# Kernel optimization log

Measured on AMD Instinct MI355X. Metric: run time of the kernel, lower is better.

## Reference

```python
import jax, jax.numpy as jnp
import numpy as np

D = 4096       # hidden_size
H = 32         # n_heads (tp_size=1)
DN = 128       # qk_nope_head_dim
DR = 64        # qk_rope_head_dim
DV = 128       # v_head_dim
QL = 1536      # q_lora_rank
KL = 512       # kv_lora_rank
S = 2048       # seqlen, start_pos = 0
EPS = 1e-6
SCALE = (DN + DR) ** -0.5  # softmax_scale (no yarn mscale: seqlen <= original_seq_len)
THETA = 10000.0


def _freqs(seqlen, dim, base=THETA):
    # precompute_freqs_cis without yarn correction (seqlen <= original_seq_len)
    inv = 1.0 / (base ** (np.arange(0, dim, 2, dtype=np.float32) / dim))
    f = np.outer(np.arange(seqlen, dtype=np.float32), inv)  # [S, dim//2]
    return jnp.asarray(np.cos(f)), jnp.asarray(np.sin(f))


def _rmsnorm(x, w):
    return x * jax.lax.rsqrt(jnp.mean(x * x, axis=-1, keepdims=True) + EPS) * w


def _rope(x, cos, sin):
    # x: [S, H, R]; complex rotation on consecutive pairs (view_as_complex semantics)
    S_, H_, R_ = x.shape
    xr = x.reshape(S_, H_, R_ // 2, 2)
    x0, x1 = xr[..., 0], xr[..., 1]
    c = cos[:, None, :]
    s = sin[:, None, :]
    y0 = x0 * c - x1 * s
    y1 = x0 * s + x1 * c
    return jnp.stack([y0, y1], axis=-1).reshape(S_, H_, R_)


def setup_inputs() -> dict:
    key = jax.random.key(0)
    ks = jax.random.split(key, 6)
    std = 0.02
    return {
        "x": jax.random.normal(ks[0], (S, D), jnp.float32),
        "wq_a": jax.random.normal(ks[1], (QL, D), jnp.float32) * std,
        "q_norm_w": jnp.ones((QL,), jnp.float32),
        "wq_b": jax.random.normal(ks[2], (H * (DN + DR), QL), jnp.float32) * std,
        "wkv_a": jax.random.normal(ks[3], (KL + DR, D), jnp.float32) * std,
        "kv_norm_w": jnp.ones((KL,), jnp.float32),
        "wkv_b": jax.random.normal(ks[4], (H * (DN + DV), KL), jnp.float32) * std,
        "wo": jax.random.normal(ks[5], (D, H * DV), jnp.float32) * std,
    }


def reference(x, wq_a, q_norm_w, wq_b, wkv_a, kv_norm_w, wkv_b, wo):
    cos, sin = _freqs(S, DR)

    # q path: low-rank down-proj + RMSNorm + up-proj
    q = _rmsnorm(x @ wq_a.T, q_norm_w) @ wq_b.T          # [S, H*(DN+DR)]
    q = q.reshape(S, H, DN + DR)
    q_nope, q_pe = q[..., :DN], q[..., DN:]
    q_pe = _rope(q_pe, cos, sin)                          # [S, H, DR]

    # kv path: joint latent + rope part
    kv_all = x @ wkv_a.T                                  # [S, KL+DR]
    kv = _rmsnorm(kv_all[:, :KL], kv_norm_w)              # latent kv cache [S, KL]
    k_pe = _rope(kv_all[:, None, KL:], cos, sin)[:, 0, :]  # pe cache [S, DR]

    # absorb k-up-projection into q (einsum 'shd,hdc->shc')
    wkv_b_r = wkv_b.reshape(H, DN + DV, KL)
    q_lat = jnp.einsum("shd,hdc->shc", q_nope, wkv_b_r[:, :DN])  # [S, H, KL]

    scores = (jnp.einsum("shc,tc->sht", q_lat, kv)
              + jnp.einsum("shr,tr->sht", q_pe, k_pe)) * SCALE   # [S, H, T]

    causal = jnp.arange(S)[:, None] >= jnp.arange(S)[None, :]     # [S, T]
    scores = jnp.where(causal[:, None, :], scores, -jnp.inf)
    p = jax.nn.softmax(scores, axis=-1)

    o_lat = jnp.einsum("sht,tc->shc", p, kv)                      # [S, H, KL]
    o = jnp.einsum("shc,hdc->shd", o_lat, wkv_b_r[:, DN:])        # [S, H, DV]
    return o.reshape(S, H * DV) @ wo.T                            # [S, D]
```

## Files before the change

### kernel.cpp

```cpp
#include <hip/hip_runtime.h>
#include <hip/hip_bf16.h>
#include <type_traits>

using bf16 = __hip_bfloat16;
typedef short v8s __attribute__((ext_vector_type(8)));
typedef float v4f __attribute__((ext_vector_type(4)));

#define DEV __device__ __forceinline__

constexpr float SCALE_ = 0.07216878364870322f;

DEV unsigned short bfu(float f) {
  bf16 h = __float2bfloat16(f);
  return __builtin_bit_cast(unsigned short, h);
}
DEV float b2f(short u) {
  unsigned int x = ((unsigned int)(unsigned short)u) << 16;
  return __builtin_bit_cast(float, x);
}

DEV void g2lds16(const void* g, void* l) {
  __builtin_amdgcn_global_load_lds(
      (const __attribute__((address_space(1))) unsigned int*)g,
      (__attribute__((address_space(3))) unsigned int*)l, 16, 0, 0);
}


__global__ void cast_kernel(const float* __restrict__ in, bf16* __restrict__ out, int n4) {
  int i = blockIdx.x * 256 + threadIdx.x;
  int stride = gridDim.x * 256;
  for (; i < n4; i += stride) {
    float4 v = ((const float4*)in)[i];
    ushort4 u;
    u.x = bfu(v.x); u.y = bfu(v.y); u.z = bfu(v.z); u.w = bfu(v.w);
    ((ushort4*)out)[i] = u;
  }
}

__global__ void cast_pad_kernel(const float* __restrict__ in, bf16* __restrict__ out) {
  int i = blockIdx.x * 256 + threadIdx.x;
  float4 v = make_float4(0.f, 0.f, 0.f, 0.f);
  if (i < 589824) v = ((const float4*)in)[i];
  ushort4 u;
  u.x = bfu(v.x); u.y = bfu(v.y); u.z = bfu(v.z); u.w = bfu(v.w);
  ((ushort4*)out)[i] = u;
}

__global__ void wkvbt_kernel(const float* __restrict__ wkvb, bf16* __restrict__ out) {
  int gid = blockIdx.x * 256 + threadIdx.x;
  int c8 = (gid & 63) * 8;
  int d8 = ((gid >> 6) & 15) * 8;
  int h = gid >> 10;
  float4 a[8][2];
#pragma unroll
  for (int r = 0; r < 8; ++r) {
    const float* p = wkvb + ((long)(h * 256 + d8 + r)) * 512 + c8;
    a[r][0] = *(const float4*)p;
    a[r][1] = *(const float4*)(p + 4);
  }
#pragma unroll
  for (int cc = 0; cc < 8; ++cc) {
    v8s o;
#pragma unroll
    for (int r = 0; r < 8; ++r) {
      float f = (cc < 4) ? ((const float*)&a[r][0])[cc] : ((const float*)&a[r][1])[cc - 4];
      o[r] = (short)bfu(f);
    }
    *(v8s*)(out + (long)h * 65536 + (c8 + cc) * 128 + d8) = o;
  }
}

__global__ void wkvbv_kernel(const float* __restrict__ wkvb, bf16* __restrict__ out) {
  int i = blockIdx.x * 256 + threadIdx.x;
  int c4 = i & 127, d = (i >> 7) & 127, h = i >> 14;
  float4 v = *(const float4*)(wkvb + ((long)(h * 256 + 128 + d)) * 512 + c4 * 4);
  ushort4 u;
  u.x = bfu(v.x); u.y = bfu(v.y); u.z = bfu(v.z); u.w = bfu(v.w);
  *(ushort4*)(out + ((long)(h * 128 + d)) * 512 + c4 * 4) = u;
}

__global__ void freqs_kernel(float* __restrict__ cosb, float* __restrict__ sinb) {
  int t = blockIdx.x * 256 + threadIdx.x;
  int s = t >> 5, i = t & 31;
  float inv = powf(10000.0f, -(float)(2 * i) / 64.0f);
  float f = (float)s * inv;
  cosb[t] = cosf(f);
  sinb[t] = sinf(f);
}

__global__ void rmsnorm_bf_kernel(const bf16* __restrict__ in, const float* __restrict__ w,
                                  bf16* __restrict__ out, int L, int ldin, int ldout) {
  int row = blockIdx.x;
  const bf16* x = in + (long)row * ldin;
  int L8 = L >> 3;
  float ss = 0.f;
  for (int i = threadIdx.x; i < L8; i += 256) {
    v8s v = *(const v8s*)(x + i * 8);
#pragma unroll
    for (int j = 0; j < 8; ++j) { float f = b2f(v[j]); ss += f * f; }
  }
#pragma unroll
  for (int d = 1; d < 64; d <<= 1) ss += __shfl_xor(ss, d);
  __shared__ float red[4];
  if ((threadIdx.x & 63) == 0) red[threadIdx.x >> 6] = ss;
  __syncthreads();
  float r = rsqrtf((red[0] + red[1] + red[2] + red[3]) / (float)L + 1e-6f);
  bf16* o = out + (long)row * ldout;
  for (int i = threadIdx.x; i < L8; i += 256) {
    v8s v = *(const v8s*)(x + i * 8);
    v8s u;
#pragma unroll
    for (int j = 0; j < 8; ++j)
      u[j] = (short)bfu(b2f(v[j]) * r * w[i * 8 + j]);
    *(v8s*)(o + i * 8) = u;
  }
}

__global__ void rope_kpe_kernel(const bf16* __restrict__ qakv, const float* __restrict__ cosb,
                                const float* __restrict__ sinb, bf16* __restrict__ keff) {
  int t = blockIdx.x * 256 + threadIdx.x;
  int s = t >> 5, i = t & 31;
  const bf16* p = qakv + (long)s * 2176 + 2048;
  float x0 = __bfloat162float(p[2 * i]), x1 = __bfloat162float(p[2 * i + 1]);
  float c = cosb[t], sn = sinb[t];
  bf16* o = keff + (long)s * 576 + 512;
  o[2 * i] = __float2bfloat16(x0 * c - x1 * sn);
  o[2 * i + 1] = __float2bfloat16(x0 * sn + x1 * c);
}

__global__ void rope_q_kernel(const bf16* __restrict__ qf, const float* __restrict__ cosb,
                              const float* __restrict__ sinb, bf16* __restrict__ qeff) {
  int t = blockIdx.x * 256 + threadIdx.x;
  int i = t & 31, h = (t >> 5) & 31, s = t >> 10;
  const bf16* p = qf + (long)s * 6144 + h * 192 + 128;
  float x0 = __bfloat162float(p[2 * i]), x1 = __bfloat162float(p[2 * i + 1]);
  float c = cosb[s * 32 + i], sn = sinb[s * 32 + i];
  bf16* o = qeff + (long)s * 18432 + h * 576 + 512;
  o[2 * i] = __float2bfloat16(x0 * c - x1 * sn);
  o[2 * i + 1] = __float2bfloat16(x0 * sn + x1 * c);
}

__global__ void vtrans_kernel(const bf16* __restrict__ keff, bf16* __restrict__ vT) {
  int gid = blockIdx.x * 256 + threadIdx.x;
  int t8 = (gid & 255) * 8, c8 = (gid >> 8) * 8;
  v8s in[8];
#pragma unroll
  for (int r = 0; r < 8; ++r)
    in[r] = *(const v8s*)(keff + (long)(t8 + r) * 576 + c8);
#pragma unroll
  for (int cc = 0; cc < 8; ++cc) {
    v8s o;
#pragma unroll
    for (int r = 0; r < 8; ++r) o[r] = in[r][cc];
    *(v8s*)(vT + (long)(c8 + cc) * 2048 + t8) = o;
  }
}

template <typename OutT>
__global__ __launch_bounds__(256, 3) void gemm_bt(
    const bf16* __restrict__ A, const bf16* __restrict__ B, OutT* __restrict__ C,
    int K, int lda, int ldb, int ldc, long sA, long sB, long sC) {
  __shared__ bf16 lA[8192];
  __shared__ bf16 lB[8192];
  const int tid = threadIdx.x;
  const int lane = tid & 63;
  const int w = tid >> 6, wm = w >> 1, wn = w & 1;
  const int r16 = lane & 15, hi = lane >> 4;
  const bf16* Ab = A + (long)blockIdx.z * sA + (long)blockIdx.y * 128 * lda;
  const bf16* Bb = B + (long)blockIdx.z * sB + (long)blockIdx.x * 128 * ldb;
  v4f acc[4][4] = {};
  for (int k0 = 0; k0 < K; k0 += 64) {
    __syncthreads();
#pragma unroll
    for (int it = 0; it < 4; ++it) {
      int D = it * 256 + tid;
      int row = D >> 3, sl = D & 7;
      int gs = sl ^ (row & 7);
      g2lds16(Ab + (long)row * lda + k0 + gs * 8, (char*)lA + (it * 256 + w * 64) * 16);
      g2lds16(Bb + (long)row * ldb + k0 + gs * 8, (char*)lB + (it * 256 + w * 64) * 16);
    }
    __syncthreads();
#pragma unroll
    for (int kk = 0; kk < 2; ++kk) {
      v8s af[4], bfr[4];
#pragma unroll
      for (int mi = 0; mi < 4; ++mi) {
        int r = wm * 64 + mi * 16 + r16;
        af[mi] = *(const v8s*)((const char*)lA + (r * 8 + ((kk * 4 + hi) ^ (r & 7))) * 16);
      }
#pragma unroll
      for (int ni = 0; ni < 4; ++ni) {
        int r = wn * 64 + ni * 16 + r16;
        bfr[ni] = *(const v8s*)((const char*)lB + (r * 8 + ((kk * 4 + hi) ^ (r & 7))) * 16);
      }
      __builtin_amdgcn_s_setprio(1);
#pragma unroll
      for (int mi = 0; mi < 4; ++mi)
#pragma unroll
        for (int ni = 0; ni < 4; ++ni)
          acc[mi][ni] = __builtin_amdgcn_mfma_f32_16x16x32_bf16(af[mi], bfr[ni], acc[mi][ni], 0, 0, 0);
      __builtin_amdgcn_s_setprio(0);
    }
  }
  OutT* Cb = C + (long)blockIdx.z * sC + (long)(blockIdx.y * 128) * ldc + blockIdx.x * 128;
  const int cr = hi << 2;
#pragma unroll
  for (int mi = 0; mi < 4; ++mi)
#pragma unroll
    for (int ni = 0; ni < 4; ++ni)
#pragma unroll
      for (int j = 0; j < 4; ++j) {
        long idx = (long)(wm * 64 + mi * 16 + cr + j) * ldc + wn * 64 + ni * 16 + r16;
        float v = acc[mi][ni][j];
        if constexpr (std::is_same<OutT, float>::value) Cb[idx] = v;
        else Cb[idx] = __float2bfloat16(v);
      }
}

__global__ __launch_bounds__(256, 2) void gemm_k128(
    const bf16* __restrict__ A, const bf16* __restrict__ B, bf16* __restrict__ C,
    int lda, int ldb, int ldc, long sA, long sB, long sC) {
  __shared__ bf16 lA[16384];
  __shared__ bf16 lB[16384];
  const int tid = threadIdx.x;
  const int lane = tid & 63;
  const int w = tid >> 6, wm = w >> 1, wn = w & 1;
  const int r16 = lane & 15, hi = lane >> 4;
  const bf16* Ab = A + (long)blockIdx.z * sA + (long)blockIdx.y * 128 * lda;
  const bf16* Bb = B + (long)blockIdx.z * sB + (long)blockIdx.x * 128 * ldb;
#pragma unroll
  for (int it = 0; it < 8; ++it) {
    int D = it * 256 + tid;
    int row = D >> 4, sl = D & 15;
    int gs = sl ^ (row & 7);
    g2lds16(Ab + (long)row * lda + gs * 8, (char*)lA + (it * 256 + w * 64) * 16);
    g2lds16(Bb + (long)row * ldb + gs * 8, (char*)lB + (it * 256 + w * 64) * 16);
  }
  __syncthreads();
  v4f acc[4][4] = {};
#pragma unroll
  for (int kk = 0; kk < 4; ++kk) {
    v8s af[4], bfr[4];
#pragma unroll
    for (int mi = 0; mi < 4; ++mi) {
      int r = wm * 64 + mi * 16 + r16;
      af[mi] = *(const v8s*)((const char*)lA + (r * 16 + ((kk * 4 + hi) ^ (r & 7))) * 16);
    }
#pragma unroll
    for (int ni = 0; ni < 4; ++ni) {
      int r = wn * 64 + ni * 16 + r16;
      bfr[ni] = *(const v8s*)((const char*)lB + (r * 16 + ((kk * 4 + hi) ^ (r & 7))) * 16);
    }
    __builtin_amdgcn_s_setprio(1);
#pragma unroll
    for (int mi = 0; mi < 4; ++mi)
#pragma unroll
      for (int ni = 0; ni < 4; ++ni)
        acc[mi][ni] = __builtin_amdgcn_mfma_f32_16x16x32_bf16(af[mi], bfr[ni], acc[mi][ni], 0, 0, 0);
    __builtin_amdgcn_s_setprio(0);
  }
  bf16* Cb = C + (long)blockIdx.z * sC + (long)(blockIdx.y * 128) * ldc + blockIdx.x * 128;
  const int cr = hi << 2;
#pragma unroll
  for (int mi = 0; mi < 4; ++mi)
#pragma unroll
    for (int ni = 0; ni < 4; ++ni)
#pragma unroll
      for (int j = 0; j < 4; ++j) {
        long idx = (long)(wm * 64 + mi * 16 + cr + j) * ldc + wn * 64 + ni * 16 + r16;
        Cb[idx] = __float2bfloat16(acc[mi][ni][j]);
      }
}

__device__ const signed char U_QT[24] = {15,15,7,14,14,13,13,6,12,12,11,11,5,10,10,9,9,4,8,8,3,2,1,0};
__device__ const signed char U_HF[24] = {0,1,-1,0,1,0,1,-1,0,1,0,1,-1,0,1,0,1,-1,0,1,-1,-1,-1,-1};

__global__ __launch_bounds__(512, 2) void attn_kernel(
    const bf16* __restrict__ qeff, const bf16* __restrict__ keff,
    const bf16* __restrict__ vT, bf16* __restrict__ olat,
    bf16* __restrict__ P1, float* __restrict__ mlb) {
  __shared__ __align__(16) bf16 kl[32 * 576];
  __shared__ __align__(16) bf16 vl[512 * 32];
  const int tid = threadIdx.x, lane = tid & 63, w = tid >> 6;
  const int r16 = lane & 15, hi = lane >> 4;
  const int kg = hi << 3, cr = hi << 2;
  const int h = blockIdx.x;
  const int u = blockIdx.y;
  const int qt = U_QT[u];
  const int hf = U_HF[u];
  const int nch = 4 * qt + 4;
  const int kc0 = (hf == 1) ? (nch >> 1) : 0;
  const int kc1 = (hf == 0) ? (nch >> 1) : nch;
  const int qrow = qt * 128 + w * 16 + r16;
  const int rb = r16 & 7;

  const long qbase = (long)qrow * 18432 + h * 576;
  v8s qreg[18];
#pragma unroll
  for (int kk = 0; kk < 18; ++kk)
    qreg[kk] = __builtin_nontemporal_load((const v8s*)(qeff + qbase + kk * 32 + kg));

  v4f acc[32] = {};
  float mrow = -1e30f, lrow = 0.f;

  auto stageK = [&](int t0) {
#pragma unroll
    for (int it = 0; it < 5; ++it) {
      int D = it * 512 + tid;
      if (D < 2304) {
        int row = D / 72;
        int gg = D - row * 72;
        int gs = gg ^ (row & 7);
        g2lds16(keff + (long)(t0 + row) * 576 + gs * 8,
                (char*)kl + (it * 512 + w * 64) * 16);
      }
    }
  };
  auto stageV = [&](int t0) {
#pragma unroll
    for (int it = 0; it < 4; ++it) {
      int D = it * 512 + tid;
      int row = D >> 2;
      int s = (D & 3) ^ ((row >> 1) & 3);
      g2lds16(vT + (long)row * 2048 + t0 + s * 8,
              (char*)vl + (it * 512 + w * 64) * 16);
    }
  };

  stageK(kc0 * 32);
  __syncthreads();

  for (int kc = kc0; kc < kc1; ++kc) {
    const int t0 = kc * 32;
    stageV(t0);

    const char* kb = (const char*)kl;
    v4f sf0 = {}, sf1 = {};
    __builtin_amdgcn_s_setprio(1);
#pragma unroll
    for (int kk = 0; kk < 18; ++kk) {
      int so = ((kk * 4 + hi) ^ rb) << 4;
      v8s b0 = *(const v8s*)(kb + r16 * 1152 + so);
      v8s b1 = *(const v8s*)(kb + (16 + r16) * 1152 + so);
      sf0 = __builtin_amdgcn_mfma_f32_16x16x32_bf16(b0, qreg[kk], sf0, 0, 0, 0);
      sf1 = __builtin_amdgcn_mfma_f32_16x16x32_bf16(b1, qreg[kk], sf1, 0, 0, 0);
    }
    __builtin_amdgcn_s_setprio(0);
    float s0[4], s1[4];
#pragma unroll
    for (int j = 0; j < 4; ++j) { s0[j] = sf0[j] * SCALE_; s1[j] = sf1[j] * SCALE_; }
    if (kc >= 4 * qt) {
#pragma unroll
      for (int j = 0; j < 4; ++j) {
        if (t0 + cr + j > qrow) s0[j] = -1e30f;
        if (t0 + 16 + cr + j > qrow) s1[j] = -1e30f;
      }
    }
    float mx = fmaxf(fmaxf(fmaxf(s0[0], s0[1]), fmaxf(s0[2], s0[3])),
                     fmaxf(fmaxf(s1[0], s1[1]), fmaxf(s1[2], s1[3])));
    mx = fmaxf(mx, __shfl_xor(mx, 16));
    mx = fmaxf(mx, __shfl_xor(mx, 32));
    if (!__all(mx <= mrow + 8.0f)) {
      float mn = fmaxf(mrow, mx);
      float alpha = __expf(mrow - mn);
      mrow = mn;
      lrow *= alpha;
      float af0 = __shfl(alpha, cr + 0), af1 = __shfl(alpha, cr + 1);
      float af2 = __shfl(alpha, cr + 2), af3 = __shfl(alpha, cr + 3);
#pragma unroll
      for (int c = 0; c < 32; ++c) {
        acc[c][0] *= af0; acc[c][1] *= af1; acc[c][2] *= af2; acc[c][3] *= af3;
      }
    }
    float p0[4], p1[4];
#pragma unroll
    for (int j = 0; j < 4; ++j) {
      p0[j] = __expf(s0[j] - mrow);
      p1[j] = __expf(s1[j] - mrow);
    }
    float rs = (p0[0] + p0[1]) + (p0[2] + p0[3]) + (p1[0] + p1[1]) + (p1[2] + p1[3]);
    rs += __shfl_xor(rs, 16);
    rs += __shfl_xor(rs, 32);
    lrow += rs;
    int u0 = (int)((unsigned)bfu(p0[0]) | ((unsigned)bfu(p0[1]) << 16));
    int u1 = (int)((unsigned)bfu(p0[2]) | ((unsigned)bfu(p0[3]) << 16));
    int v0 = (int)((unsigned)bfu(p1[0]) | ((unsigned)bfu(p1[1]) << 16));
    int v1 = (int)((unsigned)bfu(p1[2]) | ((unsigned)bfu(p1[3]) << 16));
    const int L1 = r16 + 32 * (hi & 1);
    const int L2 = L1 + 16;
    const bool lo = hi < 2;
    int d0a = __shfl(u0, L1), d0b = __shfl(v0, L1);
    int d1a = __shfl(u1, L1), d1b = __shfl(v1, L1);
    int d2a = __shfl(u0, L2), d2b = __shfl(v0, L2);
    int d3a = __shfl(u1, L2), d3b = __shfl(v1, L2);
    int4 pw = make_int4(lo ? d0a : d0b, lo ? d1a : d1b, lo ? d2a : d2b, lo ? d3a : d3b);
    v8s ap = __builtin_bit_cast(v8s, pw);

    __syncthreads();
    if (kc + 1 < kc1) stageK(t0 + 32);

    __builtin_amdgcn_s_setprio(1);
#pragma unroll
    for (int c = 0; c < 32; ++c) {
      const int vrow = c * 16 + r16;
      const int vsw = (hi ^ ((vrow >> 1) & 3)) << 4;
      v8s bv = *(const v8s*)((const char*)vl + vrow * 64 + vsw);
      acc[c] = __builtin_amdgcn_mfma_f32_16x16x32_bf16(ap, bv, acc[c], 0, 0, 0);
    }
    __builtin_amdgcn_s_setprio(0);
    __syncthreads();
  }
  if (hf < 0) {
    float linv0 = 1.0f / __shfl(lrow, cr + 0);
    float linv1 = 1.0f / __shfl(lrow, cr + 1);
    float linv2 = 1.0f / __shfl(lrow, cr + 2);
    float linv3 = 1.0f / __shfl(lrow, cr + 3);
    const long ob = (long)(qt * 128 + w * 16 + cr) * 16384 + h * 512 + r16;
#pragma unroll
    for (int c = 0; c < 32; ++c) {
      olat[ob + 0 * 16384 + c * 16] = __float2bfloat16(acc[c][0] * linv0);
      olat[ob + 1 * 16384 + c * 16] = __float2bfloat16(acc[c][1] * linv1);
      olat[ob + 2 * 16384 + c * 16] = __float2bfloat16(acc[c][2] * linv2);
      olat[ob + 3 * 16384 + c * 16] = __float2bfloat16(acc[c][3] * linv3);
    }
  } else {
    if (hi == 0) {
      float* mr = mlb + (((qrow - 1024) << 5) + h) * 4 + hf * 2;
      mr[0] = mrow;
      mr[1] = lrow;
    }
    bf16* dst = (hf == 0) ? olat : P1;
    const int rbase = (hf == 0) ? (qt * 128) : (qt * 128 - 1024);
    const long ob = (long)(rbase + w * 16 + cr) * 16384 + h * 512 + r16;
#pragma unroll
    for (int c = 0; c < 32; ++c) {
      dst[ob + 0 * 16384 + c * 16] = __float2bfloat16(acc[c][0]);
      dst[ob + 1 * 16384 + c * 16] = __float2bfloat16(acc[c][1]);
      dst[ob + 2 * 16384 + c * 16] = __float2bfloat16(acc[c][2]);
      dst[ob + 3 * 16384 + c * 16] = __float2bfloat16(acc[c][3]);
    }
  }
}

__global__ void combine_kernel(bf16* __restrict__ olat, const bf16* __restrict__ P1,
                               const float* __restrict__ mlb) {
  int gid = blockIdx.x * 256 + threadIdx.x;
  int cg = gid & 63, h = (gid >> 6) & 31, r = gid >> 11;
  const float* m4 = mlb + ((r << 5) + h) * 4;
  float mA = m4[0], lA = m4[1], mB = m4[2], lB = m4[3];
  float m = fmaxf(mA, mB);
  float sA = __expf(mA - m), sB = __expf(mB - m);
  float inv = 1.0f / (sA * lA + sB * lB);
  sA *= inv; sB *= inv;
  long oa = (long)(1024 + r) * 16384 + h * 512 + cg * 8;
  long ob = (long)r * 16384 + h * 512 + cg * 8;
  v8s a = *(const v8s*)(olat + oa);
  v8s b = *(const v8s*)(P1 + ob);
  v8s o;
#pragma unroll
  for (int j = 0; j < 8; ++j)
    o[j] = (short)bfu(b2f(a[j]) * sA + b2f(b[j]) * sB);
  *(v8s*)(olat + oa) = o;
}


extern "C" void kernel_launch(void* const* d_in, const int* in_sizes, int n_in,
                              void* d_out, int out_size, void* d_ws, size_t ws_size,
                              hipStream_t stream) {
  const float* x = (const float*)d_in[0];
  const float* wq_a = (const float*)d_in[1];
  const float* q_norm_w = (const float*)d_in[2];
  const float* wq_b = (const float*)d_in[3];
  const float* wkv_a = (const float*)d_in[4];
  const float* kv_norm_w = (const float*)d_in[5];
  const float* wkv_b = (const float*)d_in[6];
  const float* wo = (const float*)d_in[7];
  char* ws = (char*)d_ws;

  float* cosb  = (float*)(ws + 0);
  float* sinb  = (float*)(ws + 262144);
  bf16* qeffb  = (bf16*)(ws + 524288);
  bf16* olat   = (bf16*)(ws + 76021760);
  bf16* keff   = (bf16*)(ws + 143130624);
  bf16* vTb    = (bf16*)(ws + 145489920);
  bf16* P1b    = (bf16*)(ws + 147587072);
  float* mlb   = (float*)(ws + 181141504);
  bf16* xb     = (bf16*)(ws + 76021760);
  bf16* wqab   = (bf16*)(ws + 92798976);
  bf16* wkvabp = (bf16*)(ws + 105381888);
  bf16* qakv   = (bf16*)(ws + 110624768);
  bf16* qan    = (bf16*)(ws + 125829120);
  bf16* wqbb   = (bf16*)(ws + 76021760);
  bf16* qf     = (bf16*)(ws + 94896128);
  bf16* wkvb1t = (bf16*)(ws + 76021760);
  bf16* wkvbv  = (bf16*)(ws + 524288);
  bf16* obuf   = (bf16*)(ws + 4718592);
  bf16* wob    = (bf16*)(ws + 21495808);

  cast_kernel<<<2048, 256, 0, stream>>>(x, xb, 2097152);
  cast_kernel<<<2048, 256, 0, stream>>>(wq_a, wqab, 1572864);
  cast_pad_kernel<<<2560, 256, 0, stream>>>(wkv_a, wkvabp);
  freqs_kernel<<<256, 256, 0, stream>>>(cosb, sinb);

  gemm_bt<bf16><<<dim3(17, 16, 1), 256, 0, stream>>>(xb, wqab, qakv, 4096, 4096, 4096, 2176, 0, 0, 0);

  rmsnorm_bf_kernel<<<2048, 256, 0, stream>>>(qakv, q_norm_w, qan, 1536, 2176, 1536);
  rmsnorm_bf_kernel<<<2048, 256, 0, stream>>>(qakv + 1536, kv_norm_w, keff, 512, 2176, 576);
  rope_kpe_kernel<<<256, 256, 0, stream>>>(qakv, cosb, sinb, keff);
  vtrans_kernel<<<64, 256, 0, stream>>>(keff, vTb);

  cast_kernel<<<2048, 256, 0, stream>>>(wq_b, wqbb, 2359296);
  gemm_bt<bf16><<<dim3(48, 16, 1), 256, 0, stream>>>(qan, wqbb, qf, 1536, 1536, 1536, 6144, 0, 0, 0);

  rope_q_kernel<<<8192, 256, 0, stream>>>(qf, cosb, sinb, qeffb);
  wkvbt_kernel<<<128, 256, 0, stream>>>(wkv_b, wkvb1t);
  gemm_k128<<<dim3(4, 16, 32), 256, 0, stream>>>(qf, wkvb1t, qeffb,
      6144, 128, 18432, 192L, 65536L, 576L);

  attn_kernel<<<dim3(32, 24), 512, 0, stream>>>(qeffb, keff, vTb, olat, P1b, mlb);
  combine_kernel<<<8192, 256, 0, stream>>>(olat, P1b, mlb);

  wkvbv_kernel<<<2048, 256, 0, stream>>>(wkv_b, wkvbv);
  gemm_bt<bf16><<<dim3(1, 16, 32), 256, 0, stream>>>(olat, wkvbv, obuf,
      512, 16384, 512, 4096, 512L, 65536L, 128L);

  cast_kernel<<<2048, 256, 0, stream>>>(wo, wob, 4194304);
  gemm_bt<float><<<dim3(32, 16, 1), 256, 0, stream>>>(obuf, wob, (float*)d_out,
      4096, 4096, 4096, 4096, 0, 0, 0);
}
```

Baseline: 633.0 us.

## Rebalance causal attention work so each block processes equal key chunks

Replaces the 24-unit lookup-table schedule per head with 16 blocks per head. Each block processes exactly 34 key chunks. Even blocks take the first 34 chunks of a late query tile. Odd blocks take the remainder of that tile and then a full early query tile in a second segment. This balances causal work and fits the grid into one wave of 512 blocks, at the cost of a sequential second segment that reloads Q and restages K.

```diff
diff --git a/kernel.cpp b/kernel.cpp
--- a/kernel.cpp
+++ b/kernel.cpp
@@ -272,9 +272,6 @@
       }
 }
 
-__device__ const signed char U_QT[24] = {15,15,7,14,14,13,13,6,12,12,11,11,5,10,10,9,9,4,8,8,3,2,1,0};
-__device__ const signed char U_HF[24] = {0,1,-1,0,1,0,1,-1,0,1,0,1,-1,0,1,0,1,-1,0,1,-1,-1,-1,-1};
-
 __global__ __launch_bounds__(512, 2) void attn_kernel(
     const bf16* __restrict__ qeff, const bf16* __restrict__ keff,
     const bf16* __restrict__ vT, bf16* __restrict__ olat,
@@ -286,22 +283,7 @@
   const int kg = hi << 3, cr = hi << 2;
   const int h = blockIdx.x;
   const int u = blockIdx.y;
-  const int qt = U_QT[u];
-  const int hf = U_HF[u];
-  const int nch = 4 * qt + 4;
-  const int kc0 = (hf == 1) ? (nch >> 1) : 0;
-  const int kc1 = (hf == 0) ? (nch >> 1) : nch;
-  const int qrow = qt * 128 + w * 16 + r16;
   const int rb = r16 & 7;
-
-  const long qbase = (long)qrow * 18432 + h * 576;
-  v8s qreg[18];
-#pragma unroll
-  for (int kk = 0; kk < 18; ++kk)
-    qreg[kk] = __builtin_nontemporal_load((const v8s*)(qeff + qbase + kk * 32 + kg));
-
-  v4f acc[32] = {};
-  float mrow = -1e30f, lrow = 0.f;
 
   auto stageK = [&](int t0) {
 #pragma unroll
@@ -327,117 +309,141 @@
     }
   };
 
-  stageK(kc0 * 32);
-  __syncthreads();
-
-  for (int kc = kc0; kc < kc1; ++kc) {
-    const int t0 = kc * 32;
-    stageV(t0);
-
-    const char* kb = (const char*)kl;
-    v4f sf0 = {}, sf1 = {};
-    __builtin_amdgcn_s_setprio(1);
-#pragma unroll
-    for (int kk = 0; kk < 18; ++kk) {
-      int so = ((kk * 4 + hi) ^ rb) << 4;
-      v8s b0 = *(const v8s*)(kb + r16 * 1152 + so);
-      v8s b1 = *(const v8s*)(kb + (16 + r16) * 1152 + so);
-      sf0 = __builtin_amdgcn_mfma_f32_16x16x32_bf16(b0, qreg[kk], sf0, 0, 0, 0);
-      sf1 = __builtin_amdgcn_mfma_f32_16x16x32_bf16(b1, qreg[kk], sf1, 0, 0, 0);
-    }
-    __builtin_amdgcn_s_setprio(0);
-    float s0[4], s1[4];
-#pragma unroll
-    for (int j = 0; j < 4; ++j) { s0[j] = sf0[j] * SCALE_; s1[j] = sf1[j] * SCALE_; }
-    if (kc >= 4 * qt) {
+  v8s qreg[18];
+  v4f acc[32];
+  float mrow, lrow;
+
+  for (int seg = 0; seg < 2; ++seg) {
+    int qt, hf, kcb, kce;
+    if (seg == 0) {
+      qt = 15 - (u >> 1);
+      if (u & 1) { hf = 1; kcb = 34; kce = 4 * qt + 4; }
+      else       { hf = 0; kcb = 0;  kce = 34; }
+    } else {
+      if (!(u & 1)) break;
+      qt = u >> 1; hf = -1; kcb = 0; kce = 4 * qt + 4;
+    }
+    const int qrow = qt * 128 + w * 16 + r16;
+    const long qbase = (long)qrow * 18432 + h * 576;
+#pragma unroll
+    for (int kk = 0; kk < 18; ++kk)
+      qreg[kk] = __builtin_nontemporal_load((const v8s*)(qeff + qbase + kk * 32 + kg));
+#pragma unroll
+    for (int c = 0; c < 32; ++c) acc[c] = v4f{0.f, 0.f, 0.f, 0.f};
+    mrow = -1e30f; lrow = 0.f;
+
+    stageK(kcb * 32);
+    __syncthreads();
+
+    for (int kc = kcb; kc < kce; ++kc) {
+      const int t0 = kc * 32;
+      stageV(t0);
+
+      const char* kb = (const char*)kl;
+      v4f sf0 = {}, sf1 = {};
+      __builtin_amdgcn_s_setprio(1);
+#pragma unroll
+      for (int kk = 0; kk < 18; ++kk) {
+        int so = ((kk * 4 + hi) ^ rb) << 4;
+        v8s b0 = *(const v8s*)(kb + r16 * 1152 + so);
+        v8s b1 = *(const v8s*)(kb + (16 + r16) * 1152 + so);
+        sf0 = __builtin_amdgcn_mfma_f32_16x16x32_bf16(b0, qreg[kk], sf0, 0, 0, 0);
+        sf1 = __builtin_amdgcn_mfma_f32_16x16x32_bf16(b1, qreg[kk], sf1, 0, 0, 0);
+      }
+      __builtin_amdgcn_s_setprio(0);
+      float s0[4], s1[4];
+#pragma unroll
+      for (int j = 0; j < 4; ++j) { s0[j] = sf0[j] * SCALE_; s1[j] = sf1[j] * SCALE_; }
+      if (kc >= 4 * qt) {
+#pragma unroll
+        for (int j = 0; j < 4; ++j) {
+          if (t0 + cr + j > qrow) s0[j] = -1e30f;
+          if (t0 + 16 + cr + j > qrow) s1[j] = -1e30f;
+        }
+      }
+      float mx = fmaxf(fmaxf(fmaxf(s0[0], s0[1]), fmaxf(s0[2], s0[3])),
+                       fmaxf(fmaxf(s1[0], s1[1]), fmaxf(s1[2], s1[3])));
+      mx = fmaxf(mx, __shfl_xor(mx, 16));
+      mx = fmaxf(mx, __shfl_xor(mx, 32));
+      if (!__all(mx <= mrow + 8.0f)) {
+        float mn = fmaxf(mrow, mx);
+        float alpha = __expf(mrow - mn);
+        mrow = mn;
+        lrow *= alpha;
+        float af0 = __shfl(alpha, cr + 0), af1 = __shfl(alpha, cr + 1);
+        float af2 = __shfl(alpha, cr + 2), af3 = __shfl(alpha, cr + 3);
+#pragma unroll
+        for (int c = 0; c < 32; ++c) {
+          acc[c][0] *= af0; acc[c][1] *= af1; acc[c][2] *= af2; acc[c][3] *= af3;
+        }
+      }
+      float p0[4], p1[4];
 #pragma unroll
       for (int j = 0; j < 4; ++j) {
-        if (t0 + cr + j > qrow) s0[j] = -1e30f;
-        if (t0 + 16 + cr + j > qrow) s1[j] = -1e30f;
-      }
-    }
-    float mx = fmaxf(fmaxf(fmaxf(s0[0], s0[1]), fmaxf(s0[2], s0[3])),
-                     fmaxf(fmaxf(s1[0], s1[1]), fmaxf(s1[2], s1[3])));
-    mx = fmaxf(mx, __shfl_xor(mx, 16));
-    mx = fmaxf(mx, __shfl_xor(mx, 32));
-    if (!__all(mx <= mrow + 8.0f)) {
-      float mn = fmaxf(mrow, mx);
-      float alpha = __expf(mrow - mn);
-      mrow = mn;
-      lrow *= alpha;
-      float af0 = __shfl(alpha, cr + 0), af1 = __shfl(alpha, cr + 1);
-      float af2 = __shfl(alpha, cr + 2), af3 = __shfl(alpha, cr + 3);
+        p0[j] = __expf(s0[j] - mrow);
+        p1[j] = __expf(s1[j] - mrow);
+      }
+      float rs = (p0[0] + p0[1]) + (p0[2] + p0[3]) + (p1[0] + p1[1]) + (p1[2] + p1[3]);
+      rs += __shfl_xor(rs, 16);
+      rs += __shfl_xor(rs, 32);
+      lrow += rs;
+      int u0 = (int)((unsigned)bfu(p0[0]) | ((unsigned)bfu(p0[1]) << 16));
+      int u1 = (int)((unsigned)bfu(p0[2]) | ((unsigned)bfu(p0[3]) << 16));
+      int v0 = (int)((unsigned)bfu(p1[0]) | ((unsigned)bfu(p1[1]) << 16));
+      int v1 = (int)((unsigned)bfu(p1[2]) | ((unsigned)bfu(p1[3]) << 16));
+      const int L1 = r16 + 32 * (hi & 1);
+      const int L2 = L1 + 16;
+      const bool lo = hi < 2;
+      int d0a = __shfl(u0, L1), d0b = __shfl(v0, L1);
+      int d1a = __shfl(u1, L1), d1b = __shfl(v1, L1);
+      int d2a = __shfl(u0, L2), d2b = __shfl(v0, L2);
+      int d3a = __shfl(u1, L2), d3b = __shfl(v1, L2);
+      int4 pw = make_int4(lo ? d0a : d0b, lo ? d1a : d1b, lo ? d2a : d2b, lo ? d3a : d3b);
+      v8s ap = __builtin_bit_cast(v8s, pw);
+
+      __syncthreads();
+      if (kc + 1 < kce) stageK(t0 + 32);
+
+      __builtin_amdgcn_s_setprio(1);
 #pragma unroll
       for (int c = 0; c < 32; ++c) {
-        acc[c][0] *= af0; acc[c][1] *= af1; acc[c][2] *= af2; acc[c][3] *= af3;
-      }
-    }
-    float p0[4], p1[4];
-#pragma unroll
-    for (int j = 0; j < 4; ++j) {
-      p0[j] = __expf(s0[j] - mrow);
-      p1[j] = __expf(s1[j] - mrow);
-    }
-    float rs = (p0[0] + p0[1]) + (p0[2] + p0[3]) + (p1[0] + p1[1]) + (p1[2] + p1[3]);
-    rs += __shfl_xor(rs, 16);
-    rs += __shfl_xor(rs, 32);
-    lrow += rs;
-    int u0 = (int)((unsigned)bfu(p0[0]) | ((unsigned)bfu(p0[1]) << 16));
-    int u1 = (int)((unsigned)bfu(p0[2]) | ((unsigned)bfu(p0[3]) << 16));
-    int v0 = (int)((unsigned)bfu(p1[0]) | ((unsigned)bfu(p1[1]) << 16));
-    int v1 = (int)((unsigned)bfu(p1[2]) | ((unsigned)bfu(p1[3]) << 16));
-    const int L1 = r16 + 32 * (hi & 1);
-    const int L2 = L1 + 16;
-    const bool lo = hi < 2;
-    int d0a = __shfl(u0, L1), d0b = __shfl(v0, L1);
-    int d1a = __shfl(u1, L1), d1b = __shfl(v1, L1);
-    int d2a = __shfl(u0, L2), d2b = __shfl(v0, L2);
-    int d3a = __shfl(u1, L2), d3b = __shfl(v1, L2);
-    int4 pw = make_int4(lo ? d0a : d0b, lo ? d1a : d1b, lo ? d2a : d2b, lo ? d3a : d3b);
-    v8s ap = __builtin_bit_cast(v8s, pw);
-
-    __syncthreads();
-    if (kc + 1 < kc1) stageK(t0 + 32);
-
-    __builtin_amdgcn_s_setprio(1);
-#pragma unroll
-    for (int c = 0; c < 32; ++c) {
-      const int vrow = c * 16 + r16;
-      const int vsw = (hi ^ ((vrow >> 1) & 3)) << 4;
-      v8s bv = *(const v8s*)((const char*)vl + vrow * 64 + vsw);
-      acc[c] = __builtin_amdgcn_mfma_f32_16x16x32_bf16(ap, bv, acc[c], 0, 0, 0);
-    }
-    __builtin_amdgcn_s_setprio(0);
-    __syncthreads();
-  }
-  if (hf < 0) {
-    float linv0 = 1.0f / __shfl(lrow, cr + 0);
-    float linv1 = 1.0f / __shfl(lrow, cr + 1);
-    float linv2 = 1.0f / __shfl(lrow, cr + 2);
-    float linv3 = 1.0f / __shfl(lrow, cr + 3);
-    const long ob = (long)(qt * 128 + w * 16 + cr) * 16384 + h * 512 + r16;
-#pragma unroll
-    for (int c = 0; c < 32; ++c) {
-      olat[ob + 0 * 16384 + c * 16] = __float2bfloat16(acc[c][0] * linv0);
-      olat[ob + 1 * 16384 + c * 16] = __float2bfloat16(acc[c][1] * linv1);
-      olat[ob + 2 * 16384 + c * 16] = __float2bfloat16(acc[c][2] * linv2);
-      olat[ob + 3 * 16384 + c * 16] = __float2bfloat16(acc[c][3] * linv3);
-    }
-  } else {
-    if (hi == 0) {
-      float* mr = mlb + (((qrow - 1024) << 5) + h) * 4 + hf * 2;
-      mr[0] = mrow;
-      mr[1] = lrow;
-    }
-    bf16* dst = (hf == 0) ? olat : P1;
-    const int rbase = (hf == 0) ? (qt * 128) : (qt * 128 - 1024);
-    const long ob = (long)(rbase + w * 16 + cr) * 16384 + h * 512 + r16;
-#pragma unroll
-    for (int c = 0; c < 32; ++c) {
-      dst[ob + 0 * 16384 + c * 16] = __float2bfloat16(acc[c][0]);
-      dst[ob + 1 * 16384 + c * 16] = __float2bfloat16(acc[c][1]);
-      dst[ob + 2 * 16384 + c * 16] = __float2bfloat16(acc[c][2]);
-      dst[ob + 3 * 16384 + c * 16] = __float2bfloat16(acc[c][3]);
+        const int vrow = c * 16 + r16;
+        const int vsw = (hi ^ ((vrow >> 1) & 3)) << 4;
+        v8s bv = *(const v8s*)((const char*)vl + vrow * 64 + vsw);
+        acc[c] = __builtin_amdgcn_mfma_f32_16x16x32_bf16(ap, bv, acc[c], 0, 0, 0);
+      }
+      __builtin_amdgcn_s_setprio(0);
+      __syncthreads();
+    }
+    if (hf < 0) {
+      float linv0 = 1.0f / __shfl(lrow, cr + 0);
+      float linv1 = 1.0f / __shfl(lrow, cr + 1);
+      float linv2 = 1.0f / __shfl(lrow, cr + 2);
+      float linv3 = 1.0f / __shfl(lrow, cr + 3);
+      const long ob = (long)(qt * 128 + w * 16 + cr) * 16384 + h * 512 + r16;
+#pragma unroll
+      for (int c = 0; c < 32; ++c) {
+        olat[ob + 0 * 16384 + c * 16] = __float2bfloat16(acc[c][0] * linv0);
+        olat[ob + 1 * 16384 + c * 16] = __float2bfloat16(acc[c][1] * linv1);
+        olat[ob + 2 * 16384 + c * 16] = __float2bfloat16(acc[c][2] * linv2);
+        olat[ob + 3 * 16384 + c * 16] = __float2bfloat16(acc[c][3] * linv3);
+      }
+    } else {
+      if (hi == 0) {
+        float* mr = mlb + (((qrow - 1024) << 5) + h) * 4 + hf * 2;
+        mr[0] = mrow;
+        mr[1] = lrow;
+      }
+      bf16* dst = (hf == 0) ? olat : P1;
+      const int rbase = (hf == 0) ? (qt * 128) : (qt * 128 - 1024);
+      const long ob = (long)(rbase + w * 16 + cr) * 16384 + h * 512 + r16;
+#pragma unroll
+      for (int c = 0; c < 32; ++c) {
+        dst[ob + 0 * 16384 + c * 16] = __float2bfloat16(acc[c][0]);
+        dst[ob + 1 * 16384 + c * 16] = __float2bfloat16(acc[c][1]);
+        dst[ob + 2 * 16384 + c * 16] = __float2bfloat16(acc[c][2]);
+        dst[ob + 3 * 16384 + c * 16] = __float2bfloat16(acc[c][3]);
+      }
     }
   }
 }
@@ -517,7 +523,7 @@
   gemm_k128<<<dim3(4, 16, 32), 256, 0, stream>>>(qf, wkvb1t, qeffb,
       6144, 128, 18432, 192L, 65536L, 576L);
 
-  attn_kernel<<<dim3(32, 24), 512, 0, stream>>>(qeffb, keff, vTb, olat, P1b, mlb);
+  attn_kernel<<<dim3(32, 16), 512, 0, stream>>>(qeffb, keff, vTb, olat, P1b, mlb);
   combine_kernel<<<8192, 256, 0, stream>>>(olat, P1b, mlb);
 
   wkvbv_kernel<<<2048, 256, 0, stream>>>(wkv_b, wkvbv);
```

Measured after the change: 657.1 us. 1.04x slower.

## Add 256x256 8-phase pipelined GEMM for q up-projection and output projection

Applied to the files above, without the earlier changes.

Adds a new 512-thread GEMM kernel with 256x256 tiles, double-buffered 128KB LDS, and an 8-phase schedule. Each phase issues the next tile's global-to-LDS loads between MFMA groups, gated by explicit vmcnt waits. The wq_b up-projection and the final wo projection switch from the 128x128 gemm_bt to this kernel. The goal is higher MFMA utilisation and better overlap of loads with compute. The cost is fewer blocks, which weakens wave-level parallelism on the smaller GEMM, and the hand-tuned waitcnt values must match the issued loads exactly.

```diff
diff --git a/kernel.cpp b/kernel.cpp
--- a/kernel.cpp
+++ b/kernel.cpp
@@ -269,6 +269,112 @@
       for (int j = 0; j < 4; ++j) {
         long idx = (long)(wm * 64 + mi * 16 + cr + j) * ldc + wn * 64 + ni * 16 + r16;
         Cb[idx] = __float2bfloat16(acc[mi][ni][j]);
+      }
+}
+
+#define PH_STAGE_NONE ((void)0)
+#define PHASE8(BUF, MG, NG, STAGE_STMT, WSTR) { \
+  v8s af[4][2], bfr[2][2]; \
+  const char* sb = smem + (BUF) * 65536; \
+  _Pragma("unroll") for (int mi = 0; mi < 4; ++mi) \
+    _Pragma("unroll") for (int kk = 0; kk < 2; ++kk) { \
+      int r = wm * 128 + ((MG) * 4 + mi) * 16 + r16; \
+      af[mi][kk] = *(const v8s*)(sb + (r * 8 + ((kk * 4 + hi) ^ (r & 7))) * 16); } \
+  _Pragma("unroll") for (int ni = 0; ni < 2; ++ni) \
+    _Pragma("unroll") for (int kk = 0; kk < 2; ++kk) { \
+      int r = wn * 64 + ((NG) * 2 + ni) * 16 + r16; \
+      bfr[ni][kk] = *(const v8s*)(sb + 32768 + (r * 8 + ((kk * 4 + hi) ^ (r & 7))) * 16); } \
+  STAGE_STMT; \
+  __builtin_amdgcn_s_barrier(); \
+  __builtin_amdgcn_s_setprio(1); \
+  _Pragma("unroll") for (int mi = 0; mi < 4; ++mi) \
+    _Pragma("unroll") for (int ni = 0; ni < 2; ++ni) \
+      _Pragma("unroll") for (int kk = 0; kk < 2; ++kk) \
+        acc[(MG) * 4 + mi][(NG) * 2 + ni] = __builtin_amdgcn_mfma_f32_16x16x32_bf16( \
+            af[mi][kk], bfr[ni][kk], acc[(MG) * 4 + mi][(NG) * 2 + ni], 0, 0, 0); \
+  __builtin_amdgcn_s_setprio(0); \
+  asm volatile("s_waitcnt " WSTR ::: "memory"); \
+  __builtin_amdgcn_sched_barrier(0); \
+  __builtin_amdgcn_s_barrier(); \
+}
+
+template <typename OutT>
+__global__ __launch_bounds__(512, 2) void gemm_8p(
+    const bf16* __restrict__ A, const bf16* __restrict__ B, OutT* __restrict__ C,
+    int K, int lda, int ldb, int ldc) {
+  __shared__ __align__(16) char smem[131072];
+  const int tid = threadIdx.x, lane = tid & 63, w = tid >> 6;
+  const int r16 = lane & 15, hi = lane >> 4;
+  const int wm = w >> 2, wn = w & 3;
+  const bf16* Ab = A + (long)(blockIdx.y * 256) * lda;
+  const bf16* Bb = B + (long)(blockIdx.x * 256) * ldb;
+  const int nkt = K >> 6;
+
+  auto stageA = [&](int b, int kt, int hh) {
+#pragma unroll
+    for (int it = 0; it < 2; ++it) {
+      int d0 = it * 64 + w * 8;
+      int rowbase = ((d0 >> 6) << 7) + hh * 64 + (d0 & 63);
+      int row = rowbase + (lane >> 3);
+      int sl = lane & 7;
+      int gs = sl ^ (row & 7);
+      g2lds16(Ab + (long)row * lda + kt * 64 + gs * 8,
+              smem + b * 65536 + rowbase * 128);
+    }
+  };
+  auto stageB = [&](int b, int kt, int hh) {
+#pragma unroll
+    for (int it = 0; it < 2; ++it) {
+      int d0 = it * 64 + w * 8;
+      int rowbase = ((d0 >> 5) << 6) + hh * 32 + (d0 & 31);
+      int row = rowbase + (lane >> 3);
+      int sl = lane & 7;
+      int gs = sl ^ (row & 7);
+      g2lds16(Bb + (long)row * ldb + kt * 64 + gs * 8,
+              smem + b * 65536 + 32768 + rowbase * 128);
+    }
+  };
+
+  v4f acc[8][4] = {};
+
+  stageA(0, 0, 0); stageB(0, 0, 0); stageA(0, 0, 1); stageB(0, 0, 1);
+  stageA(1, 1, 0); stageB(1, 1, 0);
+  asm volatile("s_waitcnt vmcnt(8)" ::: "memory");
+  __builtin_amdgcn_sched_barrier(0);
+  __builtin_amdgcn_s_barrier();
+
+  int kt = 0;
+  for (; kt + 2 < nkt; kt += 2) {
+    PHASE8(0, 0, 0, stageA(1, kt + 1, 1), "vmcnt(6)")
+    PHASE8(0, 0, 1, stageB(1, kt + 1, 1), "vmcnt(10)")
+    PHASE8(0, 1, 0, stageA(0, kt + 2, 0), "vmcnt(10)")
+    PHASE8(0, 1, 1, stageB(0, kt + 2, 0), "vmcnt(8)")
+    PHASE8(1, 0, 0, stageA(0, kt + 2, 1), "vmcnt(6)")
+    PHASE8(1, 0, 1, stageB(0, kt + 2, 1), "vmcnt(10)")
+    PHASE8(1, 1, 0, stageA(1, kt + 3, 0), "vmcnt(10)")
+    PHASE8(1, 1, 1, stageB(1, kt + 3, 0), "vmcnt(8)")
+  }
+  PHASE8(0, 0, 0, stageA(1, kt + 1, 1), "vmcnt(6)")
+  PHASE8(0, 0, 1, stageB(1, kt + 1, 1), "vmcnt(10)")
+  PHASE8(0, 1, 0, PH_STAGE_NONE, "vmcnt(8)")
+  PHASE8(0, 1, 1, PH_STAGE_NONE, "vmcnt(4)")
+  PHASE8(1, 0, 0, PH_STAGE_NONE, "vmcnt(0)")
+  PHASE8(1, 0, 1, PH_STAGE_NONE, "vmcnt(2)")
+  PHASE8(1, 1, 0, PH_STAGE_NONE, "vmcnt(0)")
+  PHASE8(1, 1, 1, PH_STAGE_NONE, "vmcnt(0)")
+
+  OutT* Cb = C + (long)(blockIdx.y * 256 + wm * 128) * ldc + blockIdx.x * 256 + wn * 64;
+  const int cr = hi << 2;
+#pragma unroll
+  for (int mt = 0; mt < 8; ++mt)
+#pragma unroll
+    for (int nt = 0; nt < 4; ++nt)
+#pragma unroll
+      for (int j = 0; j < 4; ++j) {
+        long idx = (long)(mt * 16 + cr + j) * ldc + nt * 16 + r16;
+        float v = acc[mt][nt][j];
+        if constexpr (std::is_same<OutT, float>::value) Cb[idx] = v;
+        else Cb[idx] = __float2bfloat16(v);
       }
 }
 
@@ -510,7 +616,7 @@
   vtrans_kernel<<<64, 256, 0, stream>>>(keff, vTb);
 
   cast_kernel<<<2048, 256, 0, stream>>>(wq_b, wqbb, 2359296);
-  gemm_bt<bf16><<<dim3(48, 16, 1), 256, 0, stream>>>(qan, wqbb, qf, 1536, 1536, 1536, 6144, 0, 0, 0);
+  gemm_8p<bf16><<<dim3(24, 8), 512, 0, stream>>>(qan, wqbb, qf, 1536, 1536, 1536, 6144);
 
   rope_q_kernel<<<8192, 256, 0, stream>>>(qf, cosb, sinb, qeffb);
   wkvbt_kernel<<<128, 256, 0, stream>>>(wkv_b, wkvb1t);
@@ -525,6 +631,6 @@
       512, 16384, 512, 4096, 512L, 65536L, 128L);
 
   cast_kernel<<<2048, 256, 0, stream>>>(wo, wob, 4194304);
-  gemm_bt<float><<<dim3(32, 16, 1), 256, 0, stream>>>(obuf, wob, (float*)d_out,
-      4096, 4096, 4096, 4096, 0, 0, 0);
-}
+  gemm_8p<float><<<dim3(16, 8), 512, 0, stream>>>(obuf, wob, (float*)d_out,
+      4096, 4096, 4096, 4096);
+}
```

After: 650.1 us. 2.7% more time.
